# Kernel tuning notes

Measured on AMD Instinct MI355X. Metric: run time of the kernel, lower is better.

## Reference

```python
import jax, jax.numpy as jnp
import numpy as np

D_MODEL = 1024
NUM_HEADS = 16
D_K = D_MODEL // NUM_HEADS
THETA = 10000.0
MAX_SEQ_LEN = 2048
BATCH = 2
SEQ = 2048


def setup_inputs() -> dict:
    key = jax.random.key(0)
    ks = jax.random.split(key, 5)
    std = np.sqrt(2.0 / (D_MODEL + D_MODEL)).astype(np.float32)
    x = jax.random.normal(ks[0], (BATCH, SEQ, D_MODEL), dtype=jnp.float32)
    Wq = jax.random.normal(ks[1], (D_MODEL, D_MODEL), dtype=jnp.float32) * std
    Wk = jax.random.normal(ks[2], (D_MODEL, D_MODEL), dtype=jnp.float32) * std
    Wv = jax.random.normal(ks[3], (D_MODEL, D_MODEL), dtype=jnp.float32) * std
    Wo = jax.random.normal(ks[4], (D_MODEL, D_MODEL), dtype=jnp.float32) * std
    token_positions = jnp.arange(SEQ, dtype=jnp.int32)
    return {"x": x, "token_positions": token_positions,
            "Wq": Wq, "Wk": Wk, "Wv": Wv, "Wo": Wo}


def _rope_tables(positions):
    # freqs: [d_k/2]; angles: [seq, d_k/2]
    freqs = 1.0 / (THETA ** (jnp.arange(0, D_K, 2, dtype=jnp.float32) / D_K))
    angles = positions.astype(jnp.float32)[:, None] * freqs[None, :]
    return jnp.cos(angles), jnp.sin(angles)


def _apply_rope(t, cos, sin):
    # t: [b, h, s, d_k]; cos/sin: [s, d_k/2]; interleaved pair rotation
    x1 = t[..., 0::2]
    x2 = t[..., 1::2]
    r1 = x1 * cos - x2 * sin
    r2 = x1 * sin + x2 * cos
    return jnp.stack([r1, r2], axis=-1).reshape(t.shape)


def reference(x, token_positions, Wq, Wk, Wv, Wo):
    b, s, _ = x.shape
    # projections: y = x W^T
    q = jnp.einsum('bsi,oi->bso', x, Wq)
    k = jnp.einsum('bsi,oi->bso', x, Wk)
    v = jnp.einsum('bsi,oi->bso', x, Wv)
    # split heads: [b, h, s, d]
    q = q.reshape(b, s, NUM_HEADS, D_K).transpose(0, 2, 1, 3)
    k = k.reshape(b, s, NUM_HEADS, D_K).transpose(0, 2, 1, 3)
    v = v.reshape(b, s, NUM_HEADS, D_K).transpose(0, 2, 1, 3)
    cos, sin = _rope_tables(token_positions)
    q = _apply_rope(q, cos, sin)
    k = _apply_rope(k, cos, sin)
    scale = jnp.asarray(D_K, jnp.float32) ** 0.5
    scores = jnp.einsum('bhqd,bhkd->bhqk', q, k) / scale
    causal = jnp.tril(jnp.ones((s, s), dtype=bool))
    scores = jnp.where(causal, scores, -jnp.inf)
    attn = jax.nn.softmax(scores.astype(jnp.float32), axis=-1).astype(scores.dtype)
    out = jnp.einsum('bhqk,bhkd->bhqd', attn, v)
    out = out.transpose(0, 2, 1, 3).reshape(b, s, D_MODEL)
    return jnp.einsum('bsi,oi->bso', out, Wo)
```

## Files before the change

### kernel.cpp

```cpp
#include <hip/hip_runtime.h>
#include <stdint.h>

#define D_MODEL 1024
#define NH      16
#define DKH     64
#define SEQLEN  2048
#define BATCH   2
#define KDIM    1024

typedef __attribute__((ext_vector_type(8))) short          short8;
typedef __attribute__((ext_vector_type(4))) short          bf16x4;
typedef __attribute__((ext_vector_type(8))) unsigned short ushort8;
typedef __attribute__((ext_vector_type(4))) unsigned short usht4;
typedef __attribute__((ext_vector_type(4))) float          f32x4;

#define QSCALE 0.18033688011112042f

__device__ __forceinline__ unsigned short f2bf(float f) {
    union { float f; unsigned u; } v; v.f = f;
    unsigned u = v.u;
    unsigned r = (u + 0x7FFFu + ((u >> 16) & 1u)) >> 16;
    return (unsigned short)r;
}
__device__ __forceinline__ float bf2f(unsigned short h) {
    union { unsigned u; float f; } v; v.u = ((unsigned)h) << 16;
    return v.f;
}
__device__ __forceinline__ unsigned fbits(float f) {
    union { float f; unsigned u; } v; v.f = f; return v.u;
}

__device__ __forceinline__ void gload_lds16(const unsigned short* g, unsigned short* l) {
    __builtin_amdgcn_global_load_lds(
        (__attribute__((address_space(1))) void*)(g),
        (__attribute__((address_space(3))) void*)(l), 16, 0, 0);
}

__global__ void cvt_all(const float* __restrict__ X,  const float* __restrict__ Wq,
                        const float* __restrict__ Wk, const float* __restrict__ Wv,
                        const float* __restrict__ Wo,
                        unsigned short* __restrict__ Xb,  unsigned short* __restrict__ Wqb,
                        unsigned short* __restrict__ Wkb, unsigned short* __restrict__ Wvb,
                        unsigned short* __restrict__ Wob) {
    const int z = blockIdx.y;
    const float* src; unsigned short* dst; int n;
    if (z == 0)      { src = X;  dst = Xb;  n = 4194304; }
    else if (z == 1) { src = Wq; dst = Wqb; n = 1048576; }
    else if (z == 2) { src = Wk; dst = Wkb; n = 1048576; }
    else if (z == 3) { src = Wv; dst = Wvb; n = 1048576; }
    else             { src = Wo; dst = Wob; n = 1048576; }
    int i = (blockIdx.x * 256 + threadIdx.x) * 8;
    if (i >= n) return;
    float4 a = *(const float4*)(src + i);
    float4 b = *(const float4*)(src + i + 4);
    ushort8 o;
    o[0] = f2bf(a.x); o[1] = f2bf(a.y); o[2] = f2bf(a.z); o[3] = f2bf(a.w);
    o[4] = f2bf(b.x); o[5] = f2bf(b.y); o[6] = f2bf(b.z); o[7] = f2bf(b.w);
    *(ushort8*)(dst + i) = o;
}

__device__ __forceinline__ void gemm_core_128(
    const unsigned short* __restrict__ A, const unsigned short* __restrict__ W,
    unsigned short* a_lds, unsigned short* b_lds,
    int m0, int n0, f32x4 acc[4][4])
{
    const int tid  = threadIdx.x;
    const int lane = tid & 63;
    const int w    = tid >> 6;
    const int quad = lane >> 4;
    const int l16  = lane & 15;
    const int wm   = w & 1, wn = w >> 1;

    const int srow = lane >> 2;
    const int scol = (lane & 3) * 8;

    #pragma unroll
    for (int mi = 0; mi < 4; mi++)
        #pragma unroll
        for (int ni = 0; ni < 4; ni++) {
            f32x4 z = {0.f, 0.f, 0.f, 0.f};
            acc[mi][ni] = z;
        }

    for (int kk = 0; kk < KDIM; kk += 32) {
        __syncthreads();
        #pragma unroll
        for (int i = 0; i < 2; ++i) {
            int c = 2 * w + i;
            gload_lds16(A + (size_t)(m0 + c * 16 + srow) * KDIM + kk + scol, &a_lds[c * 512]);
            gload_lds16(W + (size_t)(n0 + c * 16 + srow) * KDIM + kk + scol, &b_lds[c * 512]);
        }
        __syncthreads();

        short8 af[4], bf[4];
        #pragma unroll
        for (int i = 0; i < 4; i++) {
            af[i] = *(const short8*)&a_lds[(wm * 64 + i * 16 + l16) * 32 + quad * 8];
            bf[i] = *(const short8*)&b_lds[(wn * 64 + i * 16 + l16) * 32 + quad * 8];
        }
        #pragma unroll
        for (int mi = 0; mi < 4; mi++)
            #pragma unroll
            for (int ni = 0; ni < 4; ni++)
                acc[mi][ni] = __builtin_amdgcn_mfma_f32_16x16x32_bf16(af[mi], bf[ni], acc[mi][ni], 0, 0, 0);
    }
}

__global__ __launch_bounds__(256, 2)
void gemm_qkv(const unsigned short* __restrict__ X,
              const unsigned short* __restrict__ Wq,
              const unsigned short* __restrict__ Wk,
              const unsigned short* __restrict__ Wv,
              unsigned short* __restrict__ q_ws,
              unsigned short* __restrict__ k_ws,
              unsigned short* __restrict__ v_ws)
{
    __shared__ __align__(16) unsigned short a_lds[128 * 32];
    __shared__ __align__(16) unsigned short b_lds[128 * 32];

    const int z = blockIdx.z;
    const unsigned short* W = (z == 0) ? Wq : ((z == 1) ? Wk : Wv);
    const int m0 = blockIdx.x * 128, n0 = blockIdx.y * 128;

    f32x4 acc[4][4];
    gemm_core_128(X, W, a_lds, b_lds, m0, n0, acc);

    const int lane = threadIdx.x & 63;
    const int w    = threadIdx.x >> 6;
    const int quad = lane >> 4;
    const int l16  = lane & 15;
    const int wm   = w & 1, wn = w >> 1;

    #pragma unroll
    for (int mi = 0; mi < 4; mi++)
        #pragma unroll
        for (int ni = 0; ni < 4; ni++)
            #pragma unroll
            for (int r = 0; r < 4; r++) {
                int row = m0 + wm * 64 + mi * 16 + quad * 4 + r;
                int col = n0 + wn * 64 + ni * 16 + l16;
                int b = row >> 11, s = row & 2047;
                int h = col >> 6,  d = col & 63;
                int bh = b * NH + h;
                float val = acc[mi][ni][r];
                if (z == 2) {
                    v_ws[(size_t)bh * DKH * SEQLEN + (size_t)d * SEQLEN + s] = f2bf(val);
                } else {
                    unsigned short* dst = (z == 0) ? q_ws : k_ws;
                    dst[(size_t)bh * SEQLEN * DKH + (size_t)s * DKH + d] = f2bf(val);
                }
            }
}

__global__ void rope_kernel(const int* __restrict__ pos,
                            unsigned short* __restrict__ q_ws,
                            unsigned short* __restrict__ k_ws)
{
    int i = blockIdx.x * 256 + threadIdx.x;
    int isK = i >> 19;
    unsigned short* t = isK ? k_ws : q_ws;
    float sc = isK ? 1.0f : QSCALE;
    int c   = i & 0x7FFFF;
    int bh  = c >> 14;
    int rem = c & 16383;
    int s   = rem >> 3;
    int ch  = rem & 7;
    size_t base = (size_t)bh * (SEQLEN * DKH) + (size_t)s * DKH + ch * 8;

    ushort8 v = *(ushort8*)(t + base);
    float p = (float)pos[s];
    ushort8 o;
    #pragma unroll
    for (int u = 0; u < 4; u++) {
        int j = ch * 4 + u;
        float freq = expf(-((float)(2 * j) * (1.0f / 64.0f)) * 9.210340371976184f);
        float ang = p * freq;
        float sn, cn;
        sincosf(ang, &sn, &cn);
        float x1 = bf2f(v[2 * u]);
        float x2 = bf2f(v[2 * u + 1]);
        o[2 * u]     = f2bf((x1 * cn - x2 * sn) * sc);
        o[2 * u + 1] = f2bf((x1 * sn + x2 * cn) * sc);
    }
    *(ushort8*)(t + base) = o;
}

__global__ __launch_bounds__(256, 2)
void attn_kernel(const unsigned short* __restrict__ q_ws,
                 const unsigned short* __restrict__ k_ws,
                 const unsigned short* __restrict__ v_ws,
                 unsigned short* __restrict__ ao)
{
    __shared__ __align__(16) unsigned short k_lds[128 * 72];
    __shared__ __align__(16) unsigned short v_lds[64 * 136];

    const int bh  = blockIdx.x;
    const int p   = blockIdx.y;
    const int tid = threadIdx.x, lane = tid & 63, w = tid >> 6;
    const int quad = lane >> 4, l16 = lane & 15;

    const size_t kqbase = (size_t)bh * SEQLEN * DKH;
    const size_t vbase  = (size_t)bh * DKH * SEQLEN;
    const int b = bh >> 4, h = bh & 15;

    const int krow = tid >> 3, kcol = (tid & 7) * 8;
    const int vrow = tid >> 4, vcol = (tid & 15) * 8;

    #pragma unroll
    for (int phase = 0; phase < 2; ++phase) {
        const int qt  = (phase == 0) ? (31 - p) : p;
        const int q0  = qt * 64;
        const int qw0 = q0 + w * 16;
        const int nt  = (qt + 2) >> 1;

        short8 aq[2];
        #pragma unroll
        for (int kc = 0; kc < 2; kc++)
            aq[kc] = *(const short8*)(q_ws + kqbase + (size_t)(qw0 + l16) * DKH + kc * 32 + quad * 8);

        f32x4 o_acc[4];
        #pragma unroll
        for (int df = 0; df < 4; df++) { f32x4 z = {0.f,0.f,0.f,0.f}; o_acc[df] = z; }
        float lsum = 0.f;

        ushort8 kreg[4], vreg[4];
        #pragma unroll
        for (int rr = 0; rr < 4; ++rr) {
            kreg[rr] = *(const ushort8*)(k_ws + kqbase + (size_t)(krow + rr * 32) * DKH + kcol);
            vreg[rr] = *(const ushort8*)(v_ws + vbase + (size_t)(vrow + rr * 16) * SEQLEN + vcol);
        }

        for (int t = 0; t < nt; ++t) {
            const int s0 = t * 128;
            __syncthreads();
            #pragma unroll
            for (int rr = 0; rr < 4; ++rr) {
                *(ushort8*)&k_lds[(krow + rr * 32) * 72 + kcol]  = kreg[rr];
                *(ushort8*)&v_lds[(vrow + rr * 16) * 136 + vcol] = vreg[rr];
            }
            __syncthreads();
            if (t < nt - 1) {
                int s1 = s0 + 128;
                #pragma unroll
                for (int rr = 0; rr < 4; ++rr) {
                    kreg[rr] = *(const ushort8*)(k_ws + kqbase + (size_t)(s1 + krow + rr * 32) * DKH + kcol);
                    vreg[rr] = *(const ushort8*)(v_ws + vbase + (size_t)(vrow + rr * 16) * SEQLEN + s1 + vcol);
                }
            }

            const bool diag = (t == nt - 1);
            #pragma unroll
            for (int nf = 0; nf < 8; nf++) {
                f32x4 s = {0.f,0.f,0.f,0.f};
                #pragma unroll
                for (int kc = 0; kc < 2; kc++) {
                    short8 kf = *(const short8*)&k_lds[(nf * 16 + l16) * 72 + kc * 32 + quad * 8];
                    s = __builtin_amdgcn_mfma_f32_16x16x32_bf16(kf, aq[kc], s, 0, 0, 0);
                }
                if (diag) {
                    int qg = qw0 + l16;
                    int kg = s0 + nf * 16 + quad * 4;
                    #pragma unroll
                    for (int r = 0; r < 4; r++)
                        s[r] = (kg + r <= qg) ? __builtin_amdgcn_exp2f(s[r]) : 0.f;
                } else {
                    #pragma unroll
                    for (int r = 0; r < 4; r++)
                        s[r] = __builtin_amdgcn_exp2f(s[r]);
                }
                lsum += s[0] + s[1] + s[2] + s[3];

                union { unsigned u[2]; bf16x4 v; } pk;
                pk.u[0] = __builtin_amdgcn_perm(fbits(s[1]), fbits(s[0]), 0x07060302u);
                pk.u[1] = __builtin_amdgcn_perm(fbits(s[3]), fbits(s[2]), 0x07060302u);

                #pragma unroll
                for (int df = 0; df < 4; df++) {
                    bf16x4 vf = *(const bf16x4*)&v_lds[(df * 16 + l16) * 136 + nf * 16 + quad * 4];
                    o_acc[df] = __builtin_amdgcn_mfma_f32_16x16x16bf16_1k(vf, pk.v, o_acc[df], 0, 0, 0);
                }
            }
        }

        float rs = lsum;
        rs += __shfl_xor(rs, 16);
        rs += __shfl_xor(rs, 32);
        float inv = 1.0f / rs;
        int qg = qw0 + l16;
        #pragma unroll
        for (int df = 0; df < 4; df++) {
            usht4 ov;
            #pragma unroll
            for (int r = 0; r < 4; r++) ov[r] = f2bf(o_acc[df][r] * inv);
            *(usht4*)&ao[(size_t)(b * SEQLEN + qg) * D_MODEL + h * DKH + df * 16 + quad * 4] = ov;
        }
    }
}

__global__ __launch_bounds__(256, 2)
void gemm_out(const unsigned short* __restrict__ AO,
              const unsigned short* __restrict__ Wo,
              float* __restrict__ out)
{
    __shared__ __align__(16) unsigned short a_lds[128 * 32];
    __shared__ __align__(16) unsigned short b_lds[128 * 32];

    const int m0 = blockIdx.x * 128, n0 = blockIdx.y * 128;
    f32x4 acc[4][4];
    gemm_core_128(AO, Wo, a_lds, b_lds, m0, n0, acc);

    const int lane = threadIdx.x & 63;
    const int w    = threadIdx.x >> 6;
    const int quad = lane >> 4;
    const int l16  = lane & 15;
    const int wm   = w & 1, wn = w >> 1;

    #pragma unroll
    for (int mi = 0; mi < 4; mi++)
        #pragma unroll
        for (int ni = 0; ni < 4; ni++)
            #pragma unroll
            for (int r = 0; r < 4; r++) {
                int row = m0 + wm * 64 + mi * 16 + quad * 4 + r;
                int col = n0 + wn * 64 + ni * 16 + l16;
                out[(size_t)row * D_MODEL + col] = acc[mi][ni][r];
            }
}

extern "C" void kernel_launch(void* const* d_in, const int* in_sizes, int n_in,
                              void* d_out, int out_size, void* d_ws, size_t ws_size,
                              hipStream_t stream) {
    const float* X  = (const float*)d_in[0];
    const int*   pos = (const int*)d_in[1];
    const float* Wq = (const float*)d_in[2];
    const float* Wk = (const float*)d_in[3];
    const float* Wv = (const float*)d_in[4];
    const float* Wo = (const float*)d_in[5];
    float* out = (float*)d_out;

    unsigned short* Xb  = (unsigned short*)d_ws;
    unsigned short* Wqb = Xb + 4194304;
    unsigned short* Wkb = Wqb + 1048576;
    unsigned short* Wvb = Wkb + 1048576;
    unsigned short* Wob = Wvb + 1048576;
    unsigned short* q_ws = Wob + 1048576;
    unsigned short* k_ws = q_ws + 4194304;
    unsigned short* v_ws = k_ws + 4194304;
    unsigned short* ao   = v_ws + 4194304;

    cvt_all<<<dim3(2048, 5), dim3(256), 0, stream>>>(X, Wq, Wk, Wv, Wo,
                                                     Xb, Wqb, Wkb, Wvb, Wob);
    gemm_qkv<<<dim3(32, 8, 3), dim3(256), 0, stream>>>(Xb, Wqb, Wkb, Wvb, q_ws, k_ws, v_ws);
    rope_kernel<<<dim3(4096), dim3(256), 0, stream>>>(pos, q_ws, k_ws);
    attn_kernel<<<dim3(32, 16), dim3(256), 0, stream>>>(q_ws, k_ws, v_ws, ao);
    gemm_out<<<dim3(32, 8), dim3(256), 0, stream>>>(ao, Wob, out);
}
```

Before: 190.6 us.

## Enlarge attention query tile to 128 rows, reusing K/V fragments across two subtiles

The attention kernel now has each wave handle 32 query rows as two 16-row subtiles, so a block covers 128 queries, and the grid is halved to 32x8. K and V fragments read from LDS are shared by both subtiles, which halves LDS and global K/V traffic per query. The cost is more registers (double accumulators and Q fragments), half as many blocks in flight, and more masked work on the diagonal tile.

```diff
diff --git a/kernel.cpp b/kernel.cpp
--- a/kernel.cpp
+++ b/kernel.cpp
@@ -208,20 +208,25 @@
 
     #pragma unroll
     for (int phase = 0; phase < 2; ++phase) {
-        const int qt  = (phase == 0) ? (31 - p) : p;
-        const int q0  = qt * 64;
-        const int qw0 = q0 + w * 16;
-        const int nt  = (qt + 2) >> 1;
-
-        short8 aq[2];
-        #pragma unroll
-        for (int kc = 0; kc < 2; kc++)
-            aq[kc] = *(const short8*)(q_ws + kqbase + (size_t)(qw0 + l16) * DKH + kc * 32 + quad * 8);
-
-        f32x4 o_acc[4];
-        #pragma unroll
-        for (int df = 0; df < 4; df++) { f32x4 z = {0.f,0.f,0.f,0.f}; o_acc[df] = z; }
-        float lsum = 0.f;
+        const int qt2 = (phase == 0) ? (15 - p) : p;
+        const int q0  = qt2 * 128;
+        const int nt  = qt2 + 1;
+        const int qwbase = q0 + w * 32;
+
+        short8 aq[2][2];
+        #pragma unroll
+        for (int st = 0; st < 2; st++)
+            #pragma unroll
+            for (int kc = 0; kc < 2; kc++)
+                aq[st][kc] = *(const short8*)(q_ws + kqbase +
+                    (size_t)(qwbase + st * 16 + l16) * DKH + kc * 32 + quad * 8);
+
+        f32x4 o_acc[2][4];
+        #pragma unroll
+        for (int st = 0; st < 2; st++)
+            #pragma unroll
+            for (int df = 0; df < 4; df++) { f32x4 z = {0.f,0.f,0.f,0.f}; o_acc[st][df] = z; }
+        float lsum[2] = {0.f, 0.f};
 
         ushort8 kreg[4], vreg[4];
         #pragma unroll
@@ -251,48 +256,57 @@
             const bool diag = (t == nt - 1);
             #pragma unroll
             for (int nf = 0; nf < 8; nf++) {
-                f32x4 s = {0.f,0.f,0.f,0.f};
+                short8 kf0 = *(const short8*)&k_lds[(nf * 16 + l16) * 72 + 0 * 32 + quad * 8];
+                short8 kf1 = *(const short8*)&k_lds[(nf * 16 + l16) * 72 + 1 * 32 + quad * 8];
+                bf16x4 vf[4];
                 #pragma unroll
-                for (int kc = 0; kc < 2; kc++) {
-                    short8 kf = *(const short8*)&k_lds[(nf * 16 + l16) * 72 + kc * 32 + quad * 8];
-                    s = __builtin_amdgcn_mfma_f32_16x16x32_bf16(kf, aq[kc], s, 0, 0, 0);
+                for (int df = 0; df < 4; df++)
+                    vf[df] = *(const bf16x4*)&v_lds[(df * 16 + l16) * 136 + nf * 16 + quad * 4];
+
+                #pragma unroll
+                for (int st = 0; st < 2; st++) {
+                    f32x4 s = {0.f,0.f,0.f,0.f};
+                    s = __builtin_amdgcn_mfma_f32_16x16x32_bf16(kf0, aq[st][0], s, 0, 0, 0);
+                    s = __builtin_amdgcn_mfma_f32_16x16x32_bf16(kf1, aq[st][1], s, 0, 0, 0);
+
+                    if (diag) {
+                        int qg = qwbase + st * 16 + l16;
+                        int kg = s0 + nf * 16 + quad * 4;
+                        #pragma unroll
+                        for (int r = 0; r < 4; r++)
+                            s[r] = (kg + r <= qg) ? __builtin_amdgcn_exp2f(s[r]) : 0.f;
+                    } else {
+                        #pragma unroll
+                        for (int r = 0; r < 4; r++)
+                            s[r] = __builtin_amdgcn_exp2f(s[r]);
+                    }
+                    lsum[st] += s[0] + s[1] + s[2] + s[3];
+
+                    union { unsigned u[2]; bf16x4 v; } pk;
+                    pk.u[0] = __builtin_amdgcn_perm(fbits(s[1]), fbits(s[0]), 0x07060302u);
+                    pk.u[1] = __builtin_amdgcn_perm(fbits(s[3]), fbits(s[2]), 0x07060302u);
+
+                    #pragma unroll
+                    for (int df = 0; df < 4; df++)
+                        o_acc[st][df] = __builtin_amdgcn_mfma_f32_16x16x16bf16_1k(vf[df], pk.v, o_acc[st][df], 0, 0, 0);
                 }
-                if (diag) {
-                    int qg = qw0 + l16;
-                    int kg = s0 + nf * 16 + quad * 4;
-                    #pragma unroll
-                    for (int r = 0; r < 4; r++)
-                        s[r] = (kg + r <= qg) ? __builtin_amdgcn_exp2f(s[r]) : 0.f;
-                } else {
-                    #pragma unroll
-                    for (int r = 0; r < 4; r++)
-                        s[r] = __builtin_amdgcn_exp2f(s[r]);
-                }
-                lsum += s[0] + s[1] + s[2] + s[3];
-
-                union { unsigned u[2]; bf16x4 v; } pk;
-                pk.u[0] = __builtin_amdgcn_perm(fbits(s[1]), fbits(s[0]), 0x07060302u);
-                pk.u[1] = __builtin_amdgcn_perm(fbits(s[3]), fbits(s[2]), 0x07060302u);
-
+            }
+        }
+
+        #pragma unroll
+        for (int st = 0; st < 2; st++) {
+            float rs = lsum[st];
+            rs += __shfl_xor(rs, 16);
+            rs += __shfl_xor(rs, 32);
+            float inv = 1.0f / rs;
+            int qg = qwbase + st * 16 + l16;
+            #pragma unroll
+            for (int df = 0; df < 4; df++) {
+                usht4 ov;
                 #pragma unroll
-                for (int df = 0; df < 4; df++) {
-                    bf16x4 vf = *(const bf16x4*)&v_lds[(df * 16 + l16) * 136 + nf * 16 + quad * 4];
-                    o_acc[df] = __builtin_amdgcn_mfma_f32_16x16x16bf16_1k(vf, pk.v, o_acc[df], 0, 0, 0);
-                }
-            }
-        }
-
-        float rs = lsum;
-        rs += __shfl_xor(rs, 16);
-        rs += __shfl_xor(rs, 32);
-        float inv = 1.0f / rs;
-        int qg = qw0 + l16;
-        #pragma unroll
-        for (int df = 0; df < 4; df++) {
-            usht4 ov;
-            #pragma unroll
-            for (int r = 0; r < 4; r++) ov[r] = f2bf(o_acc[df][r] * inv);
-            *(usht4*)&ao[(size_t)(b * SEQLEN + qg) * D_MODEL + h * DKH + df * 16 + quad * 4] = ov;
+                for (int r = 0; r < 4; r++) ov[r] = f2bf(o_acc[st][df][r] * inv);
+                *(usht4*)&ao[(size_t)(b * SEQLEN + qg) * D_MODEL + h * DKH + df * 16 + quad * 4] = ov;
+            }
         }
     }
 }
@@ -352,6 +366,6 @@
                                                      Xb, Wqb, Wkb, Wvb, Wob);
     gemm_qkv<<<dim3(32, 8, 3), dim3(256), 0, stream>>>(Xb, Wqb, Wkb, Wvb, q_ws, k_ws, v_ws);
     rope_kernel<<<dim3(4096), dim3(256), 0, stream>>>(pos, q_ws, k_ws);
-    attn_kernel<<<dim3(32, 16), dim3(256), 0, stream>>>(q_ws, k_ws, v_ws, ao);
+    attn_kernel<<<dim3(32, 8), dim3(256), 0, stream>>>(q_ws, k_ws, v_ws, ao);
     gemm_out<<<dim3(32, 8), dim3(256), 0, stream>>>(ao, Wob, out);
 }
```

Result: no change. 191.2 us (+0.3%).
